# Kernel optimization log

Measured on AMD Instinct MI355X. Metric: run time of the kernel, lower is better.

## Reference

```python
import jax, jax.numpy as jnp
import numpy as np

N = 10000
E = 320000
IN = 10000
HID = 128
NCLS = 2


def setup_inputs() -> dict:
    key = jax.random.key(0)
    ks = jax.random.split(key, 8)
    x = jax.random.normal(ks[0], (N, IN), dtype=jnp.float32)
    edge_index = jax.random.randint(ks[1], (2, E), 0, N, dtype=jnp.int64)
    edge_weight = jax.random.uniform(ks[2], (E,), dtype=jnp.float32)
    # GCNConv linear (no bias folding issues: PyG GCNConv uses Linear(in, out, bias=False) + separate bias)
    W_conv = jax.random.normal(ks[3], (IN, HID), dtype=jnp.float32) / np.sqrt(IN)
    b_conv = jnp.zeros((HID,), dtype=jnp.float32)
    W_lin = jax.random.normal(ks[4], (HID, NCLS), dtype=jnp.float32) / np.sqrt(HID)
    b_lin = jnp.zeros((NCLS,), dtype=jnp.float32)
    return {"x": x, "edge_index": edge_index, "edge_weight": edge_weight,
            "W_conv": W_conv, "b_conv": b_conv, "W_lin": W_lin, "b_lin": b_lin}


def reference(x, edge_index, edge_weight, W_conv, b_conv, W_lin, b_lin):
    n = x.shape[0]
    row, col = edge_index[0], edge_index[1]
    # add self loops with weight 1 (GCNConv add_self_loops=True, fill_value=1.)
    loop = jnp.arange(n, dtype=row.dtype)
    row = jnp.concatenate([row, loop])
    col = jnp.concatenate([col, loop])
    ew = jnp.concatenate([edge_weight, jnp.ones((n,), dtype=edge_weight.dtype)])
    # symmetric GCN normalization: deg from destination (col) index
    deg = jax.ops.segment_sum(ew, col, num_segments=n)
    dinv = jnp.where(deg > 0, jax.lax.rsqrt(deg), 0.0)
    norm = dinv[row] * ew * dinv[col]  # [E+N]
    # linear transform then weighted scatter-add aggregation
    h = x @ W_conv                      # [N, HID]
    msg = norm[:, None] * h[row]        # [E+N, HID] gather on source nodes
    out = jax.ops.segment_sum(msg, col, num_segments=n) + b_conv  # [N, HID]
    out = jax.nn.relu(out)
    # dropout p=0.0 is identity
    logits = out @ W_lin + b_lin        # [N, 2]
    return jax.nn.softmax(logits, axis=1)
```

## Files before the change

### kernel.cpp

```cpp
#include <hip/hip_runtime.h>
#include <hip/hip_bf16.h>
#include <math.h>

#define NN   10000
#define NE   320000
#define KK   10000
#define HID  128
#define KPAD 10048
#define MT   79
#define KITERS 157
#define NSPLIT 8

typedef __bf16 bf16x8 __attribute__((ext_vector_type(8)));
typedef float  f32x16 __attribute__((ext_vector_type(16)));

#define OFF_DINV 0u
#define OFF_FLAG 40960u
#define OFF_CNT  45056u
#define OFF_ROW  86016u
#define OFF_CUR  126976u
#define OFF_ER   262144u
#define OFF_EC   1572864u
#define OFF_CSRS 2883584u
#define OFF_CSRW 4194304u
#define OFF_H    8388608u
#define OFF_WT   13631488u

__device__ inline unsigned short f2bf(float f) {
  unsigned int v = __builtin_bit_cast(unsigned int, f);
  unsigned int lsb = (v >> 16) & 1u;
  v += 0x7fffu + lsb;
  return (unsigned short)(v >> 16);
}

__global__ __launch_bounds__(64) void k_detect(const int* __restrict__ ei,
                                               int* __restrict__ flag) {
  int t = threadIdx.x;
  int v = ei[2*t + 1];
  unsigned long long b = __ballot(v != 0);
  if (t == 0) flag[0] = (b == 0ull) ? 1 : 0;
}

__global__ __launch_bounds__(256) void k_edges(const int* __restrict__ ei,
                                               const int* __restrict__ flag,
                                               const float* __restrict__ ew,
                                               int* __restrict__ er,
                                               int* __restrict__ ec,
                                               float* __restrict__ deg,
                                               int* __restrict__ cnt) {
  int e = blockIdx.x*256 + threadIdx.x;
  if (e < NE) {
    int s = flag[0];
    int r = ei[(size_t)e << s];
    int c = ei[((size_t)(NE + e)) << s];
    er[e] = r;
    ec[e] = c;
    atomicAdd(&deg[c], ew[e]);
    atomicAdd(&cnt[c], 1);
  }
}

__global__ __launch_bounds__(256) void k_transpose(const float* __restrict__ W,
                                                   unsigned short* __restrict__ Wt) {
  __shared__ float t[32][33];
  const int tx = threadIdx.x, ty = threadIdx.y;
  const int bk = blockIdx.x, bn = blockIdx.y;
#pragma unroll
  for (int j = 0; j < 4; ++j) {
    int k = bk*32 + ty + j*8;
    int n = bn*32 + tx;
    float v = 0.0f;
    if (k < KK) v = W[(size_t)k*HID + n];
    t[ty + j*8][tx] = v;
  }
  __syncthreads();
#pragma unroll
  for (int j = 0; j < 4; ++j) {
    int n = bn*32 + ty + j*8;
    int k = bk*32 + tx;
    Wt[(size_t)n*KPAD + k] = f2bf(t[tx][ty + j*8]);
  }
}

__global__ __launch_bounds__(256) void k_scan(const int* __restrict__ cnt,
                                              int* __restrict__ rowstart,
                                              int* __restrict__ cursor,
                                              float* __restrict__ deg) {
  __shared__ int sums[256];
  const int t = threadIdx.x;
  const int CH = 40;
  const int base = t * CH;
  for (int k = 0; k < CH; ++k) {
    int i = base + k;
    if (i < NN) {
      float d = deg[i] + 1.0f;
      deg[i] = (d > 0.0f) ? (1.0f / sqrtf(d)) : 0.0f;
    }
  }
  int s = 0;
  for (int k = 0; k < CH; ++k) {
    int i = base + k;
    if (i < NN) s += cnt[i];
  }
  sums[t] = s;
  __syncthreads();
  for (int off = 1; off < 256; off <<= 1) {
    int add = (t >= off) ? sums[t - off] : 0;
    __syncthreads();
    sums[t] += add;
    __syncthreads();
  }
  int run = (t == 0) ? 0 : sums[t - 1];
  for (int k = 0; k < CH; ++k) {
    int i = base + k;
    if (i < NN) {
      rowstart[i] = run;
      cursor[i]   = run;
      run += cnt[i];
    }
  }
  if (t == 255) rowstart[NN] = run;
}

__global__ __launch_bounds__(256) void k_scatter(const int* __restrict__ er,
                                                 const int* __restrict__ ec,
                                                 const float* __restrict__ ew,
                                                 const float* __restrict__ dinv,
                                                 int* __restrict__ cursor,
                                                 int* __restrict__ csr_src,
                                                 float* __restrict__ csr_w) {
  int e = blockIdx.x*256 + threadIdx.x;
  if (e < NE) {
    int r = er[e], c = ec[e];
    int slot = atomicAdd(&cursor[c], 1);
    csr_src[slot] = r;
    csr_w[slot]   = dinv[r] * ew[e] * dinv[c];
  }
}

__global__ __launch_bounds__(256) void k_gemm(const float* __restrict__ xg,
                                              const unsigned short* __restrict__ Wt,
                                              float* __restrict__ h) {
  __shared__ unsigned short lA[128*64];
  __shared__ unsigned short lB[128*64];
  const int tid  = threadIdx.x;
  const int lane = tid & 63;
  const int w    = tid >> 6;
  const int bid  = blockIdx.x;
  const int mt   = bid % MT;
  const int kc   = bid / MT;
  const int m0   = mt * 128;
  const int it0  = (KITERS * kc) / NSPLIT;
  const int it1  = (KITERS * (kc + 1)) / NSPLIT;

  const int srow  = tid >> 3;
  const int chunk = tid & 7;
  const int swz   = chunk ^ (srow & 7);
  const int scol  = chunk * 8;

  const float* pA[4];
  const unsigned short* pB[4];
#pragma unroll
  for (int r = 0; r < 4; ++r) {
    int ga = m0 + r*32 + srow; if (ga > NN-1) ga = NN-1;
    pA[r] = xg + (size_t)ga * KK + scol;
    pB[r] = Wt + (size_t)(r*32 + srow) * KPAD + swz*8;
  }

  f32x16 acc[4];
#pragma unroll
  for (int ct = 0; ct < 4; ++ct)
#pragma unroll
    for (int q = 0; q < 16; ++q) acc[ct][q] = 0.0f;

  int co[4];
#pragma unroll
  for (int s = 0; s < 4; ++s)
    co[s] = ((((lane >> 5) + 2*s) ^ (lane & 7)) << 3);

  for (int it = it0; it < it1; ++it) {
    const int k0 = it * 64;
    __syncthreads();
#pragma unroll
    for (int r = 0; r < 4; ++r) {
      __builtin_amdgcn_global_load_lds(
          (const __attribute__((address_space(1))) unsigned int*)(pB[r] + k0),
          (__attribute__((address_space(3))) unsigned int*)(&lB[r*2048 + tid*8]),
          16, 0, 0);
    }
#pragma unroll
    for (int r = 0; r < 4; ++r) {
      float4 f0 = make_float4(0.f,0.f,0.f,0.f), f1 = f0;
      if ((k0 + scol) < KK) {
        f0 = *(const float4*)(pA[r] + k0);
        f1 = *(const float4*)(pA[r] + k0 + 4);
      }
      uint4 u;
      u.x = (unsigned)f2bf(f0.x) | ((unsigned)f2bf(f0.y) << 16);
      u.y = (unsigned)f2bf(f0.z) | ((unsigned)f2bf(f0.w) << 16);
      u.z = (unsigned)f2bf(f1.x) | ((unsigned)f2bf(f1.y) << 16);
      u.w = (unsigned)f2bf(f1.z) | ((unsigned)f2bf(f1.w) << 16);
      *((uint4*)&lA[(r*32 + srow)*64 + swz*8]) = u;
    }
    __syncthreads();

    const unsigned short* Aband = &lA[(w*32 + (lane & 31))*64];
    const unsigned short* Bband = &lB[(lane & 31)*64];
#pragma unroll
    for (int s = 0; s < 4; ++s) {
      bf16x8 a = *(const bf16x8*)(Aband + co[s]);
#pragma unroll
      for (int ct = 0; ct < 4; ++ct) {
        bf16x8 b = *(const bf16x8*)(Bband + ct*2048 + co[s]);
        acc[ct] = __builtin_amdgcn_mfma_f32_32x32x16_bf16(a, b, acc[ct], 0, 0, 0);
      }
    }
  }

#pragma unroll
  for (int ct = 0; ct < 4; ++ct) {
    int col = ct*32 + (lane & 31);
#pragma unroll
    for (int reg = 0; reg < 16; ++reg) {
      int rloc = (reg & 3) + 8*(reg >> 2) + 4*(lane >> 5);
      int row = m0 + w*32 + rloc;
      if (row < NN) atomicAdd(&h[(size_t)row*HID + col], acc[ct][reg]);
    }
  }
}

__global__ __launch_bounds__(256) void k_aggout(const int* __restrict__ rowstart,
                                                const int* __restrict__ csr_src,
                                                const float* __restrict__ csr_w,
                                                const float* __restrict__ h,
                                                const float* __restrict__ dinv,
                                                const float* __restrict__ bc,
                                                const float* __restrict__ Wl,
                                                const float* __restrict__ bl,
                                                float* __restrict__ out) {
  int i = blockIdx.x*4 + (threadIdx.x >> 6);
  if (i >= NN) return;
  int lane = threadIdx.x & 63;
  const float* hp = h + 2*lane;
  int j  = rowstart[i];
  int j1 = rowstart[i + 1];

  float ax = 0.f, ay = 0.f;
  for (; j + 3 < j1; j += 4) {
    int   s0 = csr_src[j],   s1 = csr_src[j+1], s2 = csr_src[j+2], s3 = csr_src[j+3];
    float w0 = csr_w[j],     w1 = csr_w[j+1],   w2 = csr_w[j+2],   w3 = csr_w[j+3];
    float2 a = *(const float2*)(hp + (size_t)s0*HID);
    float2 b = *(const float2*)(hp + (size_t)s1*HID);
    float2 c = *(const float2*)(hp + (size_t)s2*HID);
    float2 d = *(const float2*)(hp + (size_t)s3*HID);
    ax += w0*a.x + w1*b.x + w2*c.x + w3*d.x;
    ay += w0*a.y + w1*b.y + w2*c.y + w3*d.y;
  }
  for (; j < j1; ++j) {
    int   s0 = csr_src[j];
    float w0 = csr_w[j];
    float2 a = *(const float2*)(hp + (size_t)s0*HID);
    ax += w0*a.x; ay += w0*a.y;
  }

  float di = dinv[i], d2 = di*di;
  float2 hs = *(const float2*)(hp + (size_t)i*HID);
  float2 bb = *(const float2*)(bc + 2*lane);
  float v0 = fmaxf(ax + d2*hs.x + bb.x, 0.0f);
  float v1 = fmaxf(ay + d2*hs.y + bb.y, 0.0f);

  float4 w4 = *(const float4*)(Wl + 4*lane);
  float l0 = v0*w4.x + v1*w4.z;
  float l1 = v0*w4.y + v1*w4.w;
#pragma unroll
  for (int off = 32; off > 0; off >>= 1) {
    l0 += __shfl_down(l0, off);
    l1 += __shfl_down(l1, off);
  }
  if (lane == 0) {
    l0 += bl[0]; l1 += bl[1];
    float m  = fmaxf(l0, l1);
    float e0 = expf(l0 - m), e1 = expf(l1 - m);
    float s  = 1.0f / (e0 + e1);
    *(float2*)(out + (size_t)i*2) = make_float2(e0 * s, e1 * s);
  }
}

extern "C" void kernel_launch(void* const* d_in, const int* in_sizes, int n_in,
                              void* d_out, int out_size, void* d_ws, size_t ws_size,
                              hipStream_t stream) {
  (void)in_sizes; (void)n_in; (void)out_size; (void)ws_size;
  const float* x  = (const float*)d_in[0];
  const int*   ei = (const int*)d_in[1];
  const float* ew = (const float*)d_in[2];
  const float* Wc = (const float*)d_in[3];
  const float* bc = (const float*)d_in[4];
  const float* Wl = (const float*)d_in[5];
  const float* bl = (const float*)d_in[6];

  char* ws = (char*)d_ws;
  float* dinv = (float*)(ws + OFF_DINV);
  int*   flag = (int*)(ws + OFF_FLAG);
  int*   cnt  = (int*)(ws + OFF_CNT);
  int*   row  = (int*)(ws + OFF_ROW);
  int*   cur  = (int*)(ws + OFF_CUR);
  int*   er   = (int*)(ws + OFF_ER);
  int*   ec   = (int*)(ws + OFF_EC);
  int*   csrs = (int*)(ws + OFF_CSRS);
  float* csrw = (float*)(ws + OFF_CSRW);
  float* h    = (float*)(ws + OFF_H);
  unsigned short* Wt = (unsigned short*)(ws + OFF_WT);
  float* out = (float*)d_out;

  hipMemsetAsync(dinv, 0, NN*sizeof(float), stream);
  hipMemsetAsync(cnt,  0, NN*sizeof(int),   stream);
  hipMemsetAsync(h,    0, (size_t)NN*HID*sizeof(float), stream);

  k_detect<<<1, 64, 0, stream>>>(ei, flag);
  k_edges <<<(NE + 255)/256, 256, 0, stream>>>(ei, flag, ew, er, ec, dinv, cnt);
  k_transpose<<<dim3(KPAD/32, HID/32), dim3(32, 8), 0, stream>>>(Wc, Wt);
  k_scan<<<1, 256, 0, stream>>>(cnt, row, cur, dinv);
  k_scatter<<<(NE + 255)/256, 256, 0, stream>>>(er, ec, ew, dinv, cur, csrs, csrw);
  k_gemm<<<MT*NSPLIT, 256, 0, stream>>>(x, Wt, h);
  k_aggout<<<NN/4, 256, 0, stream>>>(row, csrs, csrw, h, dinv, bc, Wl, bl, out);
}
```

Measured before the change: 696.5 us.

## Double-buffer GEMM B tiles, load A straight to registers, fuse small preprocessing kernels

The GEMM now double-buffers the W tile in LDS and prefetches the next tile while computing the current one. The x operand is loaded straight into MFMA registers instead of going through LDS, which removes one barrier per iteration. The layout-detect kernel is folded into k_edges, and the rsqrt of the degree moves from the scan into scatter and aggregation. The scan runs with 1024 threads instead of 256. The cost is redundant rsqrt work per edge and per-lane x loads that are less coalesced, since each lane reads 32 bytes from its own row.

```diff
diff --git a/kernel.cpp b/kernel.cpp
--- a/kernel.cpp
+++ b/kernel.cpp
@@ -14,8 +14,7 @@
 typedef __bf16 bf16x8 __attribute__((ext_vector_type(8)));
 typedef float  f32x16 __attribute__((ext_vector_type(16)));
 
-#define OFF_DINV 0u
-#define OFF_FLAG 40960u
+#define OFF_DEG  0u
 #define OFF_CNT  45056u
 #define OFF_ROW  86016u
 #define OFF_CUR  126976u
@@ -33,24 +32,23 @@
   return (unsigned short)(v >> 16);
 }
 
-__global__ __launch_bounds__(64) void k_detect(const int* __restrict__ ei,
-                                               int* __restrict__ flag) {
-  int t = threadIdx.x;
-  int v = ei[2*t + 1];
-  unsigned long long b = __ballot(v != 0);
-  if (t == 0) flag[0] = (b == 0ull) ? 1 : 0;
-}
-
 __global__ __launch_bounds__(256) void k_edges(const int* __restrict__ ei,
-                                               const int* __restrict__ flag,
                                                const float* __restrict__ ew,
                                                int* __restrict__ er,
                                                int* __restrict__ ec,
                                                float* __restrict__ deg,
                                                int* __restrict__ cnt) {
-  int e = blockIdx.x*256 + threadIdx.x;
+  __shared__ int sflag;
+  const int t = threadIdx.x;
+  if (t < 64) {
+    int v = ei[2*t + 1];
+    unsigned long long b = __ballot(v != 0);
+    if (t == 0) sflag = (b == 0ull) ? 1 : 0;
+  }
+  __syncthreads();
+  const int s = sflag;
+  int e = blockIdx.x*256 + t;
   if (e < NE) {
-    int s = flag[0];
     int r = ei[(size_t)e << s];
     int c = ei[((size_t)(NE + e)) << s];
     er[e] = r;
@@ -82,35 +80,29 @@
   }
 }
 
-__global__ __launch_bounds__(256) void k_scan(const int* __restrict__ cnt,
-                                              int* __restrict__ rowstart,
-                                              int* __restrict__ cursor,
-                                              float* __restrict__ deg) {
-  __shared__ int sums[256];
+__global__ __launch_bounds__(1024) void k_scan(const int* __restrict__ cnt,
+                                               int* __restrict__ rowstart,
+                                               int* __restrict__ cursor) {
+  __shared__ int sums[1024];
   const int t = threadIdx.x;
-  const int CH = 40;
+  const int CH = 10;
   const int base = t * CH;
-  for (int k = 0; k < CH; ++k) {
-    int i = base + k;
-    if (i < NN) {
-      float d = deg[i] + 1.0f;
-      deg[i] = (d > 0.0f) ? (1.0f / sqrtf(d)) : 0.0f;
-    }
-  }
   int s = 0;
+#pragma unroll
   for (int k = 0; k < CH; ++k) {
     int i = base + k;
     if (i < NN) s += cnt[i];
   }
   sums[t] = s;
   __syncthreads();
-  for (int off = 1; off < 256; off <<= 1) {
+  for (int off = 1; off < 1024; off <<= 1) {
     int add = (t >= off) ? sums[t - off] : 0;
     __syncthreads();
     sums[t] += add;
     __syncthreads();
   }
   int run = (t == 0) ? 0 : sums[t - 1];
+#pragma unroll
   for (int k = 0; k < CH; ++k) {
     int i = base + k;
     if (i < NN) {
@@ -119,30 +111,32 @@
       run += cnt[i];
     }
   }
-  if (t == 255) rowstart[NN] = run;
+  if (t == 1023) rowstart[NN] = run;
 }
 
 __global__ __launch_bounds__(256) void k_scatter(const int* __restrict__ er,
                                                  const int* __restrict__ ec,
                                                  const float* __restrict__ ew,
-                                                 const float* __restrict__ dinv,
+                                                 const float* __restrict__ deg,
                                                  int* __restrict__ cursor,
                                                  int* __restrict__ csr_src,
                                                  float* __restrict__ csr_w) {
   int e = blockIdx.x*256 + threadIdx.x;
   if (e < NE) {
     int r = er[e], c = ec[e];
+    float dr = deg[r] + 1.0f, dc = deg[c] + 1.0f;
+    float ir = (dr > 0.0f) ? (1.0f / sqrtf(dr)) : 0.0f;
+    float ic = (dc > 0.0f) ? (1.0f / sqrtf(dc)) : 0.0f;
     int slot = atomicAdd(&cursor[c], 1);
     csr_src[slot] = r;
-    csr_w[slot]   = dinv[r] * ew[e] * dinv[c];
-  }
-}
-
-__global__ __launch_bounds__(256) void k_gemm(const float* __restrict__ xg,
-                                              const unsigned short* __restrict__ Wt,
-                                              float* __restrict__ h) {
-  __shared__ unsigned short lA[128*64];
-  __shared__ unsigned short lB[128*64];
+    csr_w[slot]   = ir * ew[e] * ic;
+  }
+}
+
+__global__ __launch_bounds__(256, 3) void k_gemm(const float* __restrict__ xg,
+                                                 const unsigned short* __restrict__ Wt,
+                                                 float* __restrict__ h) {
+  __shared__ unsigned short lB[2*128*64];
   const int tid  = threadIdx.x;
   const int lane = tid & 63;
   const int w    = tid >> 6;
@@ -156,16 +150,15 @@
   const int srow  = tid >> 3;
   const int chunk = tid & 7;
   const int swz   = chunk ^ (srow & 7);
-  const int scol  = chunk * 8;
-
-  const float* pA[4];
   const unsigned short* pB[4];
 #pragma unroll
-  for (int r = 0; r < 4; ++r) {
-    int ga = m0 + r*32 + srow; if (ga > NN-1) ga = NN-1;
-    pA[r] = xg + (size_t)ga * KK + scol;
+  for (int r = 0; r < 4; ++r)
     pB[r] = Wt + (size_t)(r*32 + srow) * KPAD + swz*8;
-  }
+
+  int arow = m0 + w*32 + (lane & 31);
+  if (arow > NN-1) arow = NN-1;
+  const int hi = lane >> 5;
+  const float* pa = xg + (size_t)arow * KK + hi*8;
 
   f32x16 acc[4];
 #pragma unroll
@@ -176,46 +169,56 @@
   int co[4];
 #pragma unroll
   for (int s = 0; s < 4; ++s)
-    co[s] = ((((lane >> 5) + 2*s) ^ (lane & 7)) << 3);
+    co[s] = (((hi + 2*s) ^ (lane & 7)) << 3);
+
+#define ISSUE_B(K0, SEL)                                                          \
+  _Pragma("unroll")                                                               \
+  for (int r = 0; r < 4; ++r) {                                                   \
+    __builtin_amdgcn_global_load_lds(                                             \
+        (const __attribute__((address_space(1))) unsigned int*)(pB[r] + (K0)),    \
+        (__attribute__((address_space(3))) unsigned int*)(&lB[(SEL)*8192 + r*2048 + tid*8]), \
+        16, 0, 0);                                                                \
+  }
+
+  ISSUE_B(it0*64, 0);
+  int nbuf = 1;
 
   for (int it = it0; it < it1; ++it) {
+    __syncthreads();
+    const int cur = nbuf ^ 1;
+    if (it + 1 < it1) { ISSUE_B((it+1)*64, nbuf); }
     const int k0 = it * 64;
-    __syncthreads();
-#pragma unroll
-    for (int r = 0; r < 4; ++r) {
-      __builtin_amdgcn_global_load_lds(
-          (const __attribute__((address_space(1))) unsigned int*)(pB[r] + k0),
-          (__attribute__((address_space(3))) unsigned int*)(&lB[r*2048 + tid*8]),
-          16, 0, 0);
-    }
-#pragma unroll
-    for (int r = 0; r < 4; ++r) {
+
+    bf16x8 af[4];
+#pragma unroll
+    for (int s = 0; s < 4; ++s) {
+      const int col = k0 + s*16 + hi*8;
       float4 f0 = make_float4(0.f,0.f,0.f,0.f), f1 = f0;
-      if ((k0 + scol) < KK) {
-        f0 = *(const float4*)(pA[r] + k0);
-        f1 = *(const float4*)(pA[r] + k0 + 4);
+      if (col < KK) {
+        f0 = *(const float4*)(pa + k0 + s*16);
+        f1 = *(const float4*)(pa + k0 + s*16 + 4);
       }
       uint4 u;
       u.x = (unsigned)f2bf(f0.x) | ((unsigned)f2bf(f0.y) << 16);
       u.y = (unsigned)f2bf(f0.z) | ((unsigned)f2bf(f0.w) << 16);
       u.z = (unsigned)f2bf(f1.x) | ((unsigned)f2bf(f1.y) << 16);
       u.w = (unsigned)f2bf(f1.z) | ((unsigned)f2bf(f1.w) << 16);
-      *((uint4*)&lA[(r*32 + srow)*64 + swz*8]) = u;
+      af[s] = __builtin_bit_cast(bf16x8, u);
     }
-    __syncthreads();
-
-    const unsigned short* Aband = &lA[(w*32 + (lane & 31))*64];
-    const unsigned short* Bband = &lB[(lane & 31)*64];
+
+    const unsigned short* Bband = &lB[cur*8192 + (lane & 31)*64];
 #pragma unroll
     for (int s = 0; s < 4; ++s) {
-      bf16x8 a = *(const bf16x8*)(Aband + co[s]);
+      bf16x8 a = af[s];
 #pragma unroll
       for (int ct = 0; ct < 4; ++ct) {
         bf16x8 b = *(const bf16x8*)(Bband + ct*2048 + co[s]);
         acc[ct] = __builtin_amdgcn_mfma_f32_32x32x16_bf16(a, b, acc[ct], 0, 0, 0);
       }
     }
-  }
+    nbuf ^= 1;
+  }
+#undef ISSUE_B
 
 #pragma unroll
   for (int ct = 0; ct < 4; ++ct) {
@@ -233,7 +236,7 @@
                                                 const int* __restrict__ csr_src,
                                                 const float* __restrict__ csr_w,
                                                 const float* __restrict__ h,
-                                                const float* __restrict__ dinv,
+                                                const float* __restrict__ deg,
                                                 const float* __restrict__ bc,
                                                 const float* __restrict__ Wl,
                                                 const float* __restrict__ bl,
@@ -263,7 +266,7 @@
     ax += w0*a.x; ay += w0*a.y;
   }
 
-  float di = dinv[i], d2 = di*di;
+  float d2 = 1.0f / (deg[i] + 1.0f);
   float2 hs = *(const float2*)(hp + (size_t)i*HID);
   float2 bb = *(const float2*)(bc + 2*lane);
   float v0 = fmaxf(ax + d2*hs.x + bb.x, 0.0f);
@@ -299,8 +302,7 @@
   const float* bl = (const float*)d_in[6];
 
   char* ws = (char*)d_ws;
-  float* dinv = (float*)(ws + OFF_DINV);
-  int*   flag = (int*)(ws + OFF_FLAG);
+  float* deg  = (float*)(ws + OFF_DEG);
   int*   cnt  = (int*)(ws + OFF_CNT);
   int*   row  = (int*)(ws + OFF_ROW);
   int*   cur  = (int*)(ws + OFF_CUR);
@@ -312,15 +314,14 @@
   unsigned short* Wt = (unsigned short*)(ws + OFF_WT);
   float* out = (float*)d_out;
 
-  hipMemsetAsync(dinv, 0, NN*sizeof(float), stream);
-  hipMemsetAsync(cnt,  0, NN*sizeof(int),   stream);
-  hipMemsetAsync(h,    0, (size_t)NN*HID*sizeof(float), stream);
-
-  k_detect<<<1, 64, 0, stream>>>(ei, flag);
-  k_edges <<<(NE + 255)/256, 256, 0, stream>>>(ei, flag, ew, er, ec, dinv, cnt);
+  hipMemsetAsync(deg, 0, NN*sizeof(float), stream);
+  hipMemsetAsync(cnt, 0, NN*sizeof(int),   stream);
+  hipMemsetAsync(h,   0, (size_t)NN*HID*sizeof(float), stream);
+
+  k_edges <<<(NE + 255)/256, 256, 0, stream>>>(ei, ew, er, ec, deg, cnt);
   k_transpose<<<dim3(KPAD/32, HID/32), dim3(32, 8), 0, stream>>>(Wc, Wt);
-  k_scan<<<1, 256, 0, stream>>>(cnt, row, cur, dinv);
-  k_scatter<<<(NE + 255)/256, 256, 0, stream>>>(er, ec, ew, dinv, cur, csrs, csrw);
+  k_scan<<<1, 1024, 0, stream>>>(cnt, row, cur);
+  k_scatter<<<(NE + 255)/256, 256, 0, stream>>>(er, ec, ew, deg, cur, csrs, csrw);
   k_gemm<<<MT*NSPLIT, 256, 0, stream>>>(x, Wt, h);
-  k_aggout<<<NN/4, 256, 0, stream>>>(row, csrs, csrw, h, dinv, bc, Wl, bl, out);
-}
+  k_aggout<<<NN/4, 256, 0, stream>>>(row, csrs, csrw, h, deg, bc, Wl, bl, out);
+}
```

Result: faster. 673.3 us (-3.3%).
